# Kernel optimization log

Measured on AMD Instinct MI355X. Metric: run time of the kernel, lower is better.

The kernel has to match this reference:

```python
import jax, jax.numpy as jnp
import numpy as np

K = 3        # kernel_size
STRIDE = 1
PAD = 1
DIL = 1


def setup_inputs() -> dict:
    key = jax.random.key(0)
    ks = jax.random.split(key, 5)
    B, C, H, W, O = 4, 64, 128, 128, 64
    x = jax.random.normal(ks[0], (B, C, H, W), jnp.float32)
    # small offset-conv weights -> offsets of a few pixels (realistic trained regime)
    offset_w = jax.random.normal(ks[1], (2 * K * K, C, K, K), jnp.float32) * 0.01
    offset_b = jax.random.normal(ks[2], (2 * K * K,), jnp.float32) * 0.01
    weight = jax.random.normal(ks[3], (O, C, K, K), jnp.float32)
    bias = jax.random.normal(ks[4], (O,), jnp.float32)
    return {"x": x, "offset_w": offset_w, "offset_b": offset_b,
            "weight": weight, "bias": bias}


def _conv2d(x, w, b):
    y = jax.lax.conv_general_dilated(
        x, w, window_strides=(STRIDE, STRIDE),
        padding=[(PAD, PAD), (PAD, PAD)],
        dimension_numbers=("NCHW", "OIHW", "NCHW"))
    return y + b[None, :, None, None]


def _deform_conv2d(x, offset, weight, bias):
    B, C, H, W = x.shape
    O = weight.shape[0]
    KK = K * K
    Ho, Wo = offset.shape[2], offset.shape[3]
    # offset channels ordered (y, x) per kernel tap: [B, KK, 2, Ho, Wo]
    off = offset.reshape(B, KK, 2, Ho, Wo)
    kyy, kxx = jnp.meshgrid(jnp.arange(K) * DIL, jnp.arange(K) * DIL, indexing="ij")
    kyy = kyy.reshape(KK).astype(x.dtype)
    kxx = kxx.reshape(KK).astype(x.dtype)
    base_y = (jnp.arange(Ho) * STRIDE - PAD).astype(x.dtype)
    base_x = (jnp.arange(Wo) * STRIDE - PAD).astype(x.dtype)
    # sampling positions [B, KK, Ho, Wo]
    py = base_y[None, None, :, None] + kyy[None, :, None, None] + off[:, :, 0]
    px = base_x[None, None, None, :] + kxx[None, :, None, None] + off[:, :, 1]

    y0 = jnp.floor(py); x0 = jnp.floor(px)
    y1 = y0 + 1.0;      x1 = x0 + 1.0
    wy1 = py - y0; wy0 = 1.0 - wy1
    wx1 = px - x0; wx0 = 1.0 - wx1

    xf = x.reshape(B, C, H * W)

    def corner(yc, xc):
        valid = (yc >= 0) & (yc < H) & (xc >= 0) & (xc < W)  # zero padding outside
        idx = (jnp.clip(yc, 0, H - 1) * W + jnp.clip(xc, 0, W - 1)).astype(jnp.int32)
        g = jax.vmap(lambda xb, ib: xb[:, ib.reshape(-1)])(xf, idx)  # [B, C, KK*Ho*Wo]
        g = g.reshape(B, C, KK, Ho, Wo)
        return g * valid[:, None].astype(x.dtype)

    val = (corner(y0, x0) * (wy0 * wx0)[:, None]
         + corner(y0, x1) * (wy0 * wx1)[:, None]
         + corner(y1, x0) * (wy1 * wx0)[:, None]
         + corner(y1, x1) * (wy1 * wx1)[:, None])  # [B, C, KK, Ho, Wo]

    out = jnp.einsum("bckhw,ock->bohw", val, weight.reshape(O, C, KK))
    return out + bias[None, :, None, None]


def reference(x, offset_w, offset_b, weight, bias):
    offset = _conv2d(x, offset_w, offset_b)
    return _deform_conv2d(x, offset, weight, bias)
```

## Files before the change

### kernel.cpp

```cpp
#include <hip/hip_runtime.h>

#define B_   4
#define C_   64
#define O_   64
#define H_   128
#define W_   128
#define HW_  (H_ * W_)
#define KK_  9
#define M_   18

typedef short  short8  __attribute__((ext_vector_type(8)));
typedef float  floatx4 __attribute__((ext_vector_type(4)));
typedef unsigned short ushort4v __attribute__((ext_vector_type(4)));
typedef unsigned short ushort8v __attribute__((ext_vector_type(8)));

static __device__ __forceinline__ unsigned short f2bf(float f) {
    unsigned int u = __float_as_uint(f);
    u += 0x7FFFu + ((u >> 16) & 1u);
    return (unsigned short)(u >> 16);
}
static __device__ __forceinline__ float bf2f(unsigned short s) {
    return __uint_as_float((unsigned int)s << 16);
}

__global__ __launch_bounds__(256) void prep(
        const float* __restrict__ x, const float* __restrict__ w,
        const float* __restrict__ ow, unsigned short* __restrict__ xT,
        unsigned short* __restrict__ wtbf, unsigned short* __restrict__ owtbf) {
    const int blk = blockIdx.x;
    if (blk < 512) {
        __shared__ unsigned short T[128][72];
        const int tid = threadIdx.x;
        const int y = blk & (H_ - 1);
        const int b = blk >> 7;
        const float* xby = x + (size_t)b * C_ * HW_ + y * W_;
        for (int i = tid; i < C_ * W_; i += 256) {
            const int c = i >> 7, xc = i & 127;
            T[xc][c] = f2bf(xby[(size_t)c * HW_ + xc]);
        }
        __syncthreads();
        unsigned short* dst = xT + (size_t)b * (4 * HW_ * 16) + y * (W_ * 16);
        for (int j = tid; j < 2048; j += 256) {
            const int g  = j >> 9;
            const int x8 = (j >> 2) & 127;
            const int c0 = (j & 3) * 4;
            const ushort4v pk = *(const ushort4v*)&T[x8][g * 16 + c0];
            *(ushort4v*)&dst[(size_t)g * (HW_ * 16) + x8 * 16 + c0] = pk;
        }
    } else if (blk < 530) {
        const int i = (blk - 512) * 256 + threadIdx.x;
        const int lane = i & 63, rest = i >> 6;
        const int ot = rest & 3, cks = rest >> 2;
        const int chunk = cks / 6, ks = cks % 6;
        const int o = ot * 16 + (lane & 15);
        const int kbase = chunk * 192 + ks * 32 + (lane >> 4) * 8;
        ushort8v pk;
        #pragma unroll
        for (int j = 0; j < 8; ++j) {
            const int k = kbase + j;
            pk[j] = f2bf(w[o * 576 + (k & 63) * 9 + (k >> 6)]);
        }
        *(ushort8v*)&wtbf[(size_t)i * 8] = pk;
    } else {
        const int i = (blk - 530) * 256 + threadIdx.x;
        const int lane = i & 63, rest = i >> 6;
        const int tile = rest & 1, tks = rest >> 1;
        const int tap = tks >> 1, ks = tks & 1;
        const int m = tile * 16 + (lane & 15);
        const int cb = ks * 32 + (lane >> 4) * 8;
        ushort8v pk;
        #pragma unroll
        for (int j = 0; j < 8; ++j)
            pk[j] = (m < M_) ? f2bf(ow[m * 576 + (cb + j) * 9 + tap])
                             : (unsigned short)0;
        *(ushort8v*)&owtbf[(size_t)i * 8] = pk;
    }
}

__global__ __launch_bounds__(256, 4) void dcn_fused(
        const unsigned short* __restrict__ xT,
        const unsigned short* __restrict__ owtbf, const float* __restrict__ ob,
        const unsigned short* __restrict__ wtbf, const float* __restrict__ bias,
        float* __restrict__ out) {
    __shared__ union {
        unsigned short P[3][66][72];
        struct {
            unsigned short vals[64][192];
            float offs[4][M_][16];
        } bv;
    } u;

    const int tid    = threadIdx.x;
    const int lane   = tid & 63;
    const int wslot  = __builtin_amdgcn_readfirstlane(tid >> 6);
    const int lane15 = lane & 15;
    const int quad   = lane >> 4;

    const int g    = blockIdx.x;
    const int xcd  = g & 7;
    const int slot = g >> 3;
    const int ho   = xcd * 16 + (slot >> 3);
    const int b    = (slot >> 1) & 3;
    const int wo_base = (slot & 1) << 6;

    const unsigned short* xTb = xT + (size_t)b * (4 * HW_ * 16);

    #pragma unroll
    for (int it = 0; it < 3; ++it) {
        const int t  = it * 4 + wslot;
        const int ky = t >> 2, cgp = t & 3;
        const int y  = ho - 1 + ky;
        const bool yv = (unsigned)y < (unsigned)H_;
        const unsigned short* src = xTb + (size_t)cgp * (HW_ * 16) + y * (W_ * 16);
        #pragma unroll
        for (int pass = 0; pass < 2; ++pass) {
            const int r = pass * 64 + lane;
            if (r < 66) {
                const int cx = wo_base + r - 1;
                ushort8v p0 = {0, 0, 0, 0, 0, 0, 0, 0};
                ushort8v p1 = {0, 0, 0, 0, 0, 0, 0, 0};
                if (yv && (unsigned)cx < (unsigned)W_) {
                    p0 = *(const ushort8v*)&src[cx * 16];
                    p1 = *(const ushort8v*)&src[cx * 16 + 8];
                }
                *(ushort8v*)&u.P[ky][r][cgp * 16]     = p0;
                *(ushort8v*)&u.P[ky][r][cgp * 16 + 8] = p1;
            }
        }
    }
    __syncthreads();

    floatx4 oa0 = (floatx4){0.f, 0.f, 0.f, 0.f};
    floatx4 oa1 = (floatx4){0.f, 0.f, 0.f, 0.f};
    {
        const int pxt = wslot;
        #pragma unroll
        for (int ky = 0; ky < 3; ++ky) {
            #pragma unroll
            for (int kx = 0; kx < 3; ++kx) {
                const int tap = ky * 3 + kx;
                #pragma unroll
                for (int ks = 0; ks < 2; ++ks) {
                    const int kk = ks * 32 + quad * 8;
                    const short8 af =
                        *(const short8*)&u.P[ky][pxt * 16 + lane15 + kx][kk];
                    const int fb = ((tap * 2 + ks) * 2) * 64 + lane;
                    const short8 bf0 = *(const short8*)&owtbf[(size_t)fb * 8];
                    const short8 bf1 =
                        *(const short8*)&owtbf[(size_t)(fb + 64) * 8];
                    oa0 = __builtin_amdgcn_mfma_f32_16x16x32_bf16(af, bf0, oa0, 0, 0, 0);
                    oa1 = __builtin_amdgcn_mfma_f32_16x16x32_bf16(af, bf1, oa1, 0, 0, 0);
                }
            }
        }
    }
    __syncthreads();

    {
        const float ob0 = ob[lane15];
        #pragma unroll
        for (int r = 0; r < 4; ++r) oa0[r] += ob0;
        *(floatx4*)&u.bv.offs[wslot][lane15][quad * 4] = oa0;
        if (lane15 < 2) {
            const float ob1 = ob[16 + lane15];
            #pragma unroll
            for (int r = 0; r < 4; ++r) oa1[r] += ob1;
            *(floatx4*)&u.bv.offs[wslot][16 + lane15][quad * 4] = oa1;
        }
    }

    const int cg4  = lane & 3;
    const int px16 = lane >> 2;
    const int row  = wslot * 16 + px16;
    floatx4 acc[4];
    #pragma unroll
    for (int t = 0; t < 4; ++t) acc[t] = (floatx4){0.f, 0.f, 0.f, 0.f};

    for (int chunk = 0; chunk < 3; ++chunk) {
        #pragma unroll
        for (int tl = 0; tl < 3; ++tl) {
            const int k  = chunk * 3 + tl;
            const int ky = k / 3, kx = k % 3;
            const float offy = u.bv.offs[wslot][2 * k][px16];
            const float offx = u.bv.offs[wslot][2 * k + 1][px16];
            const float py  = (float)(ho - 1 + ky) + offy;
            const float pxx = (float)(wo_base - 1 + kx + wslot * 16 + px16) + offx;
            const float fy = floorf(py), fx = floorf(pxx);
            const int y0 = (int)fy, x0 = (int)fx;
            const int y1 = y0 + 1,  x1 = x0 + 1;
            const float wy1 = py - fy,  wy0 = 1.f - wy1;
            const float wx1 = pxx - fx, wx0 = 1.f - wx1;
            const bool y0v = (unsigned)y0 < (unsigned)H_;
            const bool y1v = (unsigned)y1 < (unsigned)H_;
            const bool x0v = (unsigned)x0 < (unsigned)W_;
            const bool x1v = (unsigned)x1 < (unsigned)W_;
            const float w00 = (y0v && x0v) ? wy0 * wx0 : 0.f;
            const float w01 = (y0v && x1v) ? wy0 * wx1 : 0.f;
            const float w10 = (y1v && x0v) ? wy1 * wx0 : 0.f;
            const float w11 = (y1v && x1v) ? wy1 * wx1 : 0.f;
            const int ry0 = min(max(y0, 0), H_ - 1);
            const int ry1 = min(max(y1, 0), H_ - 1);
            const int cx0 = min(max(x0, 0), W_ - 1);
            const int cx1 = min(max(x1, 0), W_ - 1);
            const int b00 = (ry0 * W_ + cx0) * 16 + cg4 * 4;
            const int b01 = (ry0 * W_ + cx1) * 16 + cg4 * 4;
            const int b10 = (ry1 * W_ + cx0) * 16 + cg4 * 4;
            const int b11 = (ry1 * W_ + cx1) * 16 + cg4 * 4;
            #pragma unroll
            for (int cgrp = 0; cgrp < 4; ++cgrp) {
                const unsigned short* xp = xTb + (size_t)cgrp * (HW_ * 16);
                const ushort4v q00 = *(const ushort4v*)&xp[b00];
                const ushort4v q01 = *(const ushort4v*)&xp[b01];
                const ushort4v q10 = *(const ushort4v*)&xp[b10];
                const ushort4v q11 = *(const ushort4v*)&xp[b11];
                ushort4v pk;
                #pragma unroll
                for (int q = 0; q < 4; ++q) {
                    const float val = bf2f(q00[q]) * w00 + bf2f(q01[q]) * w01
                                    + bf2f(q10[q]) * w10 + bf2f(q11[q]) * w11;
                    pk[q] = f2bf(val);
                }
                const int cidx =
                    tl * 8 + (((cgrp << 1) + (cg4 >> 1)) ^ (px16 & 7));
                *(ushort4v*)&u.bv.vals[row][cidx * 8 + (cg4 & 1) * 4] = pk;
            }
        }

        #pragma unroll
        for (int ks = 0; ks < 6; ++ks) {
            const int c16 = ks * 4 + quad;
            const int ca  = c16 >> 3;
            const int cbr = (c16 & 7) ^ (lane15 & 7);
            const short8 afrag = *(const short8*)
                &u.bv.vals[wslot * 16 + lane15][(ca * 8 + cbr) * 8];
            #pragma unroll
            for (int t = 0; t < 4; ++t) {
                const short8 bfrag = *(const short8*)
                    &wtbf[(size_t)(((chunk * 6 + ks) * 4 + t) * 64 + lane) * 8];
                acc[t] = __builtin_amdgcn_mfma_f32_16x16x32_bf16(
                             afrag, bfrag, acc[t], 0, 0, 0);
            }
        }
    }

    float* epw = (float*)&u.bv.vals[wslot * 16][0];
    #pragma unroll
    for (int t = 0; t < 4; ++t)
        #pragma unroll
        for (int r = 0; r < 4; ++r)
            epw[(t * 16 + lane15) * 17 + quad * 4 + r] = acc[t][r];

    const int wo = wo_base + wslot * 16 + lane15;
    #pragma unroll
    for (int i = 0; i < 16; ++i) {
        const int o = i * 4 + quad;
        out[(size_t)(b * O_ + o) * HW_ + ho * W_ + wo] =
            epw[o * 17 + lane15] + bias[o];
    }
}

extern "C" void kernel_launch(void* const* d_in, const int* in_sizes, int n_in,
                              void* d_out, int out_size, void* d_ws, size_t ws_size,
                              hipStream_t stream) {
    const float* x    = (const float*)d_in[0];
    const float* ow   = (const float*)d_in[1];
    const float* ob   = (const float*)d_in[2];
    const float* w    = (const float*)d_in[3];
    const float* bias = (const float*)d_in[4];
    float* out = (float*)d_out;

    unsigned short* wtbf  = (unsigned short*)d_ws;
    unsigned short* owtbf = wtbf + 4608 * 8;
    unsigned short* xT    = owtbf + 2304 * 8;

    prep<<<539, 256, 0, stream>>>(x, w, ow, xT, wtbf, owtbf);
    dcn_fused<<<B_ * H_ * (W_ / 64), 256, 0, stream>>>(xT, owtbf, ob, wtbf, bias, out);
}
```

Measured before the change: 115.5 us.

## Halve pixel tile per block and split channel reduction across wave pairs

Each block now covers 32 output pixels instead of 64, doubling the grid. Two waves share each 16-pixel tile, with each wave gathering half the channel groups and running half the K-slices of the main MFMA reduction. Partial accumulators are then exchanged and summed through shared memory, and each wave writes half the output channels. LDS per block shrinks and launch bounds allow 8 blocks per CU to raise occupancy and parallelism. The cost is that the offset conv is now computed redundantly by both waves of a pair, plus two extra barriers and the LDS reduction.

```diff
diff --git a/kernel.cpp b/kernel.cpp
--- a/kernel.cpp
+++ b/kernel.cpp
@@ -77,17 +77,21 @@
     }
 }
 
-__global__ __launch_bounds__(256, 4) void dcn_fused(
+__global__ __launch_bounds__(256, 8) void dcn_fused(
         const unsigned short* __restrict__ xT,
         const unsigned short* __restrict__ owtbf, const float* __restrict__ ob,
         const unsigned short* __restrict__ wtbf, const float* __restrict__ bias,
         float* __restrict__ out) {
     __shared__ union {
-        unsigned short P[3][66][72];
+        unsigned short P[3][34][72];
         struct {
-            unsigned short vals[64][192];
+            unsigned short vals[32][192];
             float offs[4][M_][16];
         } bv;
+        struct {
+            float ex[2][2][32][16];
+            float epw[2][2][32][17];
+        } ep;
     } u;
 
     const int tid    = threadIdx.x;
@@ -95,13 +99,16 @@
     const int wslot  = __builtin_amdgcn_readfirstlane(tid >> 6);
     const int lane15 = lane & 15;
     const int quad   = lane >> 4;
+    const int p      = wslot & 1;
+    const int h      = wslot >> 1;
 
     const int g    = blockIdx.x;
     const int xcd  = g & 7;
     const int slot = g >> 3;
-    const int ho   = xcd * 16 + (slot >> 3);
-    const int b    = (slot >> 1) & 3;
-    const int wo_base = (slot & 1) << 6;
+    const int ho   = xcd * 16 + (slot >> 4);
+    const int rest = slot & 15;
+    const int b    = rest >> 2;
+    const int wo_base = (rest & 3) << 5;
 
     const unsigned short* xTb = xT + (size_t)b * (4 * HW_ * 16);
 
@@ -112,45 +119,38 @@
         const int y  = ho - 1 + ky;
         const bool yv = (unsigned)y < (unsigned)H_;
         const unsigned short* src = xTb + (size_t)cgp * (HW_ * 16) + y * (W_ * 16);
-        #pragma unroll
-        for (int pass = 0; pass < 2; ++pass) {
-            const int r = pass * 64 + lane;
-            if (r < 66) {
-                const int cx = wo_base + r - 1;
-                ushort8v p0 = {0, 0, 0, 0, 0, 0, 0, 0};
-                ushort8v p1 = {0, 0, 0, 0, 0, 0, 0, 0};
-                if (yv && (unsigned)cx < (unsigned)W_) {
-                    p0 = *(const ushort8v*)&src[cx * 16];
-                    p1 = *(const ushort8v*)&src[cx * 16 + 8];
-                }
-                *(ushort8v*)&u.P[ky][r][cgp * 16]     = p0;
-                *(ushort8v*)&u.P[ky][r][cgp * 16 + 8] = p1;
-            }
+        const int r = lane;
+        if (r < 34) {
+            const int cx = wo_base + r - 1;
+            ushort8v p0 = {0, 0, 0, 0, 0, 0, 0, 0};
+            ushort8v p1 = {0, 0, 0, 0, 0, 0, 0, 0};
+            if (yv && (unsigned)cx < (unsigned)W_) {
+                p0 = *(const ushort8v*)&src[cx * 16];
+                p1 = *(const ushort8v*)&src[cx * 16 + 8];
+            }
+            *(ushort8v*)&u.P[ky][r][cgp * 16]     = p0;
+            *(ushort8v*)&u.P[ky][r][cgp * 16 + 8] = p1;
         }
     }
     __syncthreads();
 
     floatx4 oa0 = (floatx4){0.f, 0.f, 0.f, 0.f};
     floatx4 oa1 = (floatx4){0.f, 0.f, 0.f, 0.f};
-    {
-        const int pxt = wslot;
-        #pragma unroll
-        for (int ky = 0; ky < 3; ++ky) {
-            #pragma unroll
-            for (int kx = 0; kx < 3; ++kx) {
-                const int tap = ky * 3 + kx;
-                #pragma unroll
-                for (int ks = 0; ks < 2; ++ks) {
-                    const int kk = ks * 32 + quad * 8;
-                    const short8 af =
-                        *(const short8*)&u.P[ky][pxt * 16 + lane15 + kx][kk];
-                    const int fb = ((tap * 2 + ks) * 2) * 64 + lane;
-                    const short8 bf0 = *(const short8*)&owtbf[(size_t)fb * 8];
-                    const short8 bf1 =
-                        *(const short8*)&owtbf[(size_t)(fb + 64) * 8];
-                    oa0 = __builtin_amdgcn_mfma_f32_16x16x32_bf16(af, bf0, oa0, 0, 0, 0);
-                    oa1 = __builtin_amdgcn_mfma_f32_16x16x32_bf16(af, bf1, oa1, 0, 0, 0);
-                }
+    #pragma unroll
+    for (int ky = 0; ky < 3; ++ky) {
+        #pragma unroll
+        for (int kx = 0; kx < 3; ++kx) {
+            const int tap = ky * 3 + kx;
+            #pragma unroll
+            for (int ks = 0; ks < 2; ++ks) {
+                const int kk = ks * 32 + quad * 8;
+                const short8 af =
+                    *(const short8*)&u.P[ky][p * 16 + lane15 + kx][kk];
+                const int fb = ((tap * 2 + ks) * 2) * 64 + lane;
+                const short8 bf0 = *(const short8*)&owtbf[(size_t)fb * 8];
+                const short8 bf1 = *(const short8*)&owtbf[(size_t)(fb + 64) * 8];
+                oa0 = __builtin_amdgcn_mfma_f32_16x16x32_bf16(af, bf0, oa0, 0, 0, 0);
+                oa1 = __builtin_amdgcn_mfma_f32_16x16x32_bf16(af, bf1, oa1, 0, 0, 0);
             }
         }
     }
@@ -171,7 +171,7 @@
 
     const int cg4  = lane & 3;
     const int px16 = lane >> 2;
-    const int row  = wslot * 16 + px16;
+    const int row  = p * 16 + px16;
     floatx4 acc[4];
     #pragma unroll
     for (int t = 0; t < 4; ++t) acc[t] = (floatx4){0.f, 0.f, 0.f, 0.f};
@@ -184,7 +184,7 @@
             const float offy = u.bv.offs[wslot][2 * k][px16];
             const float offx = u.bv.offs[wslot][2 * k + 1][px16];
             const float py  = (float)(ho - 1 + ky) + offy;
-            const float pxx = (float)(wo_base - 1 + kx + wslot * 16 + px16) + offx;
+            const float pxx = (float)(wo_base - 1 + kx + p * 16 + px16) + offx;
             const float fy = floorf(py), fx = floorf(pxx);
             const int y0 = (int)fy, x0 = (int)fx;
             const int y1 = y0 + 1,  x1 = x0 + 1;
@@ -207,7 +207,8 @@
             const int b10 = (ry1 * W_ + cx0) * 16 + cg4 * 4;
             const int b11 = (ry1 * W_ + cx1) * 16 + cg4 * 4;
             #pragma unroll
-            for (int cgrp = 0; cgrp < 4; ++cgrp) {
+            for (int cgl = 0; cgl < 2; ++cgl) {
+                const int cgrp = h * 2 + cgl;
                 const unsigned short* xp = xTb + (size_t)cgrp * (HW_ * 16);
                 const ushort4v q00 = *(const ushort4v*)&xp[b00];
                 const ushort4v q01 = *(const ushort4v*)&xp[b01];
@@ -227,35 +228,49 @@
         }
 
         #pragma unroll
-        for (int ks = 0; ks < 6; ++ks) {
-            const int c16 = ks * 4 + quad;
+        for (int sl = 0; sl < 3; ++sl) {
+            const int s   = sl * 2 + h;
+            const int c16 = s * 4 + quad;
             const int ca  = c16 >> 3;
             const int cbr = (c16 & 7) ^ (lane15 & 7);
             const short8 afrag = *(const short8*)
-                &u.bv.vals[wslot * 16 + lane15][(ca * 8 + cbr) * 8];
+                &u.bv.vals[p * 16 + lane15][(ca * 8 + cbr) * 8];
             #pragma unroll
             for (int t = 0; t < 4; ++t) {
                 const short8 bfrag = *(const short8*)
-                    &wtbf[(size_t)(((chunk * 6 + ks) * 4 + t) * 64 + lane) * 8];
+                    &wtbf[(size_t)(((chunk * 6 + s) * 4 + t) * 64 + lane) * 8];
                 acc[t] = __builtin_amdgcn_mfma_f32_16x16x32_bf16(
                              afrag, bfrag, acc[t], 0, 0, 0);
             }
         }
     }
 
-    float* epw = (float*)&u.bv.vals[wslot * 16][0];
-    #pragma unroll
-    for (int t = 0; t < 4; ++t)
+    __syncthreads();
+    #pragma unroll
+    for (int tl = 0; tl < 2; ++tl) {
+        const int t = 2 * (1 - h) + tl;
+        *(floatx4*)&u.ep.ex[p][1 - h][tl * 16 + lane15][quad * 4] = acc[t];
+    }
+    __syncthreads();
+    #pragma unroll
+    for (int tl = 0; tl < 2; ++tl) {
+        const int t = 2 * h + tl;
+        const floatx4 part =
+            *(const floatx4*)&u.ep.ex[p][h][tl * 16 + lane15][quad * 4];
+        #pragma unroll
+        for (int r = 0; r < 4; ++r) acc[t][r] += part[r];
         #pragma unroll
         for (int r = 0; r < 4; ++r)
-            epw[(t * 16 + lane15) * 17 + quad * 4 + r] = acc[t][r];
-
-    const int wo = wo_base + wslot * 16 + lane15;
-    #pragma unroll
-    for (int i = 0; i < 16; ++i) {
-        const int o = i * 4 + quad;
+            u.ep.epw[p][h][tl * 16 + lane15][quad * 4 + r] = acc[t][r];
+    }
+
+    const int wo = wo_base + p * 16 + lane15;
+    #pragma unroll
+    for (int i = 0; i < 8; ++i) {
+        const int o_local = i * 4 + quad;
+        const int o = h * 32 + o_local;
         out[(size_t)(b * O_ + o) * HW_ + ho * W_ + wo] =
-            epw[o * 17 + lane15] + bias[o];
+            u.ep.epw[p][h][o_local][lane15] + bias[o];
     }
 }
 
@@ -274,5 +289,5 @@
     unsigned short* xT    = owtbf + 2304 * 8;
 
     prep<<<539, 256, 0, stream>>>(x, w, ow, xT, wtbf, owtbf);
-    dcn_fused<<<B_ * H_ * (W_ / 64), 256, 0, stream>>>(xT, owtbf, ob, wtbf, bias, out);
-}
+    dcn_fused<<<B_ * H_ * (W_ / 32), 256, 0, stream>>>(xT, owtbf, ob, wtbf, bias, out);
+}
```

After: 119.4 us. 1.03x slower.

## Feed bilinear-sampled values straight into MFMA A fragments, bypassing LDS staging

Applied to the files above, without the earlier changes.

Each lane now owns one output pixel (lane&15) and eight consecutive channels, matching the MFMA 16x16x32 A-operand layout. The bilinearly interpolated bf16 values go straight into the matrix multiply instead of being written to a swizzled shared-memory tile and read back. This removes the LDS round trip and its address math, and the per-wave offsets buffer is moved out of the union. In exchange, the four lane quads of each pixel repeat the sampling-coordinate math, and the gathers become 16-byte loads per corner.

```diff
diff --git a/kernel.cpp b/kernel.cpp
--- a/kernel.cpp
+++ b/kernel.cpp
@@ -84,11 +84,9 @@
         float* __restrict__ out) {
     __shared__ union {
         unsigned short P[3][66][72];
-        struct {
-            unsigned short vals[64][192];
-            float offs[4][M_][16];
-        } bv;
+        float ep[4][64][17];
     } u;
+    __shared__ float offs[4][M_][16];
 
     const int tid    = threadIdx.x;
     const int lane   = tid & 63;
@@ -154,24 +152,22 @@
             }
         }
     }
-    __syncthreads();
-
     {
         const float ob0 = ob[lane15];
         #pragma unroll
         for (int r = 0; r < 4; ++r) oa0[r] += ob0;
-        *(floatx4*)&u.bv.offs[wslot][lane15][quad * 4] = oa0;
+        *(floatx4*)&offs[wslot][lane15][quad * 4] = oa0;
         if (lane15 < 2) {
             const float ob1 = ob[16 + lane15];
             #pragma unroll
             for (int r = 0; r < 4; ++r) oa1[r] += ob1;
-            *(floatx4*)&u.bv.offs[wslot][16 + lane15][quad * 4] = oa1;
-        }
-    }
-
-    const int cg4  = lane & 3;
-    const int px16 = lane >> 2;
-    const int row  = wslot * 16 + px16;
+            *(floatx4*)&offs[wslot][16 + lane15][quad * 4] = oa1;
+        }
+    }
+    __syncthreads();
+
+    const int p   = wslot;
+    const int pxg = p * 16 + lane15;
     floatx4 acc[4];
     #pragma unroll
     for (int t = 0; t < 4; ++t) acc[t] = (floatx4){0.f, 0.f, 0.f, 0.f};
@@ -181,10 +177,10 @@
         for (int tl = 0; tl < 3; ++tl) {
             const int k  = chunk * 3 + tl;
             const int ky = k / 3, kx = k % 3;
-            const float offy = u.bv.offs[wslot][2 * k][px16];
-            const float offx = u.bv.offs[wslot][2 * k + 1][px16];
+            const float offy = offs[wslot][2 * k][lane15];
+            const float offx = offs[wslot][2 * k + 1][lane15];
             const float py  = (float)(ho - 1 + ky) + offy;
-            const float pxx = (float)(wo_base - 1 + kx + wslot * 16 + px16) + offx;
+            const float pxx = (float)(wo_base - 1 + kx + pxg) + offx;
             const float fy = floorf(py), fx = floorf(pxx);
             const int y0 = (int)fy, x0 = (int)fx;
             const int y1 = y0 + 1,  x1 = x0 + 1;
@@ -202,55 +198,45 @@
             const int ry1 = min(max(y1, 0), H_ - 1);
             const int cx0 = min(max(x0, 0), W_ - 1);
             const int cx1 = min(max(x1, 0), W_ - 1);
-            const int b00 = (ry0 * W_ + cx0) * 16 + cg4 * 4;
-            const int b01 = (ry0 * W_ + cx1) * 16 + cg4 * 4;
-            const int b10 = (ry1 * W_ + cx0) * 16 + cg4 * 4;
-            const int b11 = (ry1 * W_ + cx1) * 16 + cg4 * 4;
+            const int a00 = (ry0 * W_ + cx0) * 16;
+            const int a01 = (ry0 * W_ + cx1) * 16;
+            const int a10 = (ry1 * W_ + cx0) * 16;
+            const int a11 = (ry1 * W_ + cx1) * 16;
             #pragma unroll
-            for (int cgrp = 0; cgrp < 4; ++cgrp) {
-                const unsigned short* xp = xTb + (size_t)cgrp * (HW_ * 16);
-                const ushort4v q00 = *(const ushort4v*)&xp[b00];
-                const ushort4v q01 = *(const ushort4v*)&xp[b01];
-                const ushort4v q10 = *(const ushort4v*)&xp[b10];
-                const ushort4v q11 = *(const ushort4v*)&xp[b11];
-                ushort4v pk;
+            for (int chalf = 0; chalf < 2; ++chalf) {
+                const int c0 = chalf * 32 + quad * 8;
+                const unsigned short* xp =
+                    xTb + (size_t)(c0 >> 4) * (HW_ * 16) + (c0 & 8);
+                const ushort8v q00 = *(const ushort8v*)&xp[a00];
+                const ushort8v q01 = *(const ushort8v*)&xp[a01];
+                const ushort8v q10 = *(const ushort8v*)&xp[a10];
+                const ushort8v q11 = *(const ushort8v*)&xp[a11];
+                ushort8v pk;
                 #pragma unroll
-                for (int q = 0; q < 4; ++q) {
-                    const float val = bf2f(q00[q]) * w00 + bf2f(q01[q]) * w01
-                                    + bf2f(q10[q]) * w10 + bf2f(q11[q]) * w11;
-                    pk[q] = f2bf(val);
+                for (int j = 0; j < 8; ++j)
+                    pk[j] = f2bf(bf2f(q00[j]) * w00 + bf2f(q01[j]) * w01
+                               + bf2f(q10[j]) * w10 + bf2f(q11[j]) * w11);
+                const short8 af = *(const short8*)&pk;
+                const int cks = chunk * 6 + tl * 2 + chalf;
+                #pragma unroll
+                for (int t = 0; t < 4; ++t) {
+                    const short8 bfrag = *(const short8*)
+                        &wtbf[(size_t)((cks * 4 + t) * 64 + lane) * 8];
+                    acc[t] = __builtin_amdgcn_mfma_f32_16x16x32_bf16(
+                                 af, bfrag, acc[t], 0, 0, 0);
                 }
-                const int cidx =
-                    tl * 8 + (((cgrp << 1) + (cg4 >> 1)) ^ (px16 & 7));
-                *(ushort4v*)&u.bv.vals[row][cidx * 8 + (cg4 & 1) * 4] = pk;
             }
         }
-
-        #pragma unroll
-        for (int ks = 0; ks < 6; ++ks) {
-            const int c16 = ks * 4 + quad;
-            const int ca  = c16 >> 3;
-            const int cbr = (c16 & 7) ^ (lane15 & 7);
-            const short8 afrag = *(const short8*)
-                &u.bv.vals[wslot * 16 + lane15][(ca * 8 + cbr) * 8];
-            #pragma unroll
-            for (int t = 0; t < 4; ++t) {
-                const short8 bfrag = *(const short8*)
-                    &wtbf[(size_t)(((chunk * 6 + ks) * 4 + t) * 64 + lane) * 8];
-                acc[t] = __builtin_amdgcn_mfma_f32_16x16x32_bf16(
-                             afrag, bfrag, acc[t], 0, 0, 0);
-            }
-        }
-    }
-
-    float* epw = (float*)&u.bv.vals[wslot * 16][0];
+    }
+
+    float* epw = &u.ep[wslot][0][0];
     #pragma unroll
     for (int t = 0; t < 4; ++t)
         #pragma unroll
         for (int r = 0; r < 4; ++r)
             epw[(t * 16 + lane15) * 17 + quad * 4 + r] = acc[t][r];
 
-    const int wo = wo_base + wslot * 16 + lane15;
+    const int wo = wo_base + p * 16 + lane15;
     #pragma unroll
     for (int i = 0; i < 16; ++i) {
         const int o = i * 4 + quad;
```

Result: faster. 110.7 us (-4.1%).
